# Optimization experiments

Measured on AMD Instinct MI355X. Metric: run time of the kernel, lower is better.

The kernel has to match this reference:

```python
import jax, jax.numpy as jnp
import numpy as np

T, B, N, F = 128, 8, 32, 128
H = 256  # hidden channels
DEG = 8


def setup_inputs() -> dict:
    key = jax.random.key(0)
    ks = jax.random.split(key, 8)
    data = jax.random.normal(ks[0], (T, B, N, F), jnp.float32)
    all_ohs = jax.random.normal(ks[1], (T, B, N, 8), jnp.float32)
    n0 = B * N * T
    n1 = B * N * (T // 2)
    edge_index0 = jax.random.randint(ks[2], (2, n0 * DEG), 0, n0)
    edge_index1 = jax.random.randint(ks[3], (2, n1 * DEG), 0, n1)
    def init(k, shape, fan):
        return jax.random.normal(k, shape, jnp.float32) / np.float32(np.sqrt(fan))
    W0 = init(ks[4], (2 * F, H), 2 * F); b0 = jnp.zeros((H,), jnp.float32)
    Wc0 = init(ks[5], (H, H, 5), H * 5); bc0 = jnp.zeros((H,), jnp.float32)
    W1 = init(ks[6], (2 * H, H), 2 * H); b1 = jnp.zeros((H,), jnp.float32)
    Wc1 = init(ks[7], (H, H, 5), H * 5); bc1 = jnp.zeros((H,), jnp.float32)
    return dict(data=data, all_ohs=all_ohs,
                edge_index0=edge_index0, edge_index1=edge_index1,
                W0=W0, b0=b0, Wc0=Wc0, bc0=bc0,
                W1=W1, b1=b1, Wc1=Wc1, bc1=bc1)


def edge_conv(x, edge_index, W, b):
    # PyG EdgeConv: out_i = max_{(j->i)} relu(Linear(cat[x_i, x_j - x_i]))
    src, dst = edge_index[0], edge_index[1]
    x_i = x[dst]           # [E, C] target features
    x_j = x[src]           # [E, C] source features
    msg = jax.nn.relu(jnp.concatenate([x_i, x_j - x_i], axis=-1) @ W + b)
    out = jax.ops.segment_max(msg, dst, num_segments=x.shape[0])
    return jnp.where(jnp.isneginf(out), 0.0, out)  # empty segments -> 0 (PyG fill)


def temp_conv(x, Wc, bc):
    # x: [BN, C, L]; Conv1d(k=5, pad=2) + relu + MaxPool1d(2)
    y = jax.lax.conv_general_dilated(x, Wc, (1,), [(2, 2)],
                                     dimension_numbers=('NCH', 'OIH', 'NCH'))
    y = jax.nn.relu(y + bc[None, :, None])
    L2 = y.shape[-1] // 2
    y = y[..., : L2 * 2].reshape(y.shape[0], y.shape[1], L2, 2)
    return jnp.max(y, axis=-1)


def reference(data, all_ohs, edge_index0, edge_index1,
              W0, b0, Wc0, bc0, W1, b1, Wc1, bc1):
    # 'fast' path, context=False: all_ohs unused beyond reshape
    length = data.shape[0]
    x = data.reshape(T, B * N, F).transpose(1, 0, 2).reshape(-1, F)  # [BN*T, F]
    layers = ((edge_index0, W0, b0, Wc0, bc0),
              (edge_index1, W1, b1, Wc1, bc1))
    for ei, W, b, Wc, bc in layers:
        x = edge_conv(x, ei, W, b)                       # [BN*length, C]
        x = x.reshape(-1, length, x.shape[-1])           # [BN, length, C]
        x = x.transpose(0, 2, 1)                         # [BN, C, length]
        x = temp_conv(x, Wc, bc)                         # [BN, C, length//2]
        length = x.shape[2]
        C = x.shape[1]
        x = x.transpose(0, 2, 1).reshape(-1, C)          # [BN*length, C]
    return x
```

## Files before the change

### kernel.cpp

```cpp
#include <hip/hip_runtime.h>
#include <hip/hip_bf16.h>
#include <math.h>

#define T0 128
#define BN 256
#define Ff 128
#define Hh 256
#define NODE0 32768
#define E0 262144
#define T1 64
#define NODE1 16384
#define E1 131072
#define CAP 48

typedef __attribute__((ext_vector_type(8))) short bhalf8;
typedef __attribute__((ext_vector_type(4))) float floatx4;
typedef __attribute__((ext_vector_type(16))) float floatx16;

__device__ __forceinline__ unsigned short f2bf(float x) {
  union { float f; unsigned u; } v; v.f = x;
  unsigned r = v.u + 0x7fff + ((v.u >> 16) & 1);
  return (unsigned short)(r >> 16);
}
__device__ __forceinline__ float bf2f(unsigned short b) {
  union { unsigned u; float f; } v; v.u = ((unsigned)b) << 16;
  return v.f;
}
__device__ __forceinline__ void max2(float& mlo, float& mhi, int p) {
  union { unsigned u; float f; } lo, hi;
  lo.u = ((unsigned)p) << 16;
  hi.u = ((unsigned)p) & 0xffff0000u;
  mlo = fmaxf(mlo, lo.f);
  mhi = fmaxf(mhi, hi.f);
}

__global__ void k_prepfill(const float* __restrict__ data, unsigned short* __restrict__ X0b,
                           const float* __restrict__ W0, unsigned short* __restrict__ Wbot0,
                           unsigned short* __restrict__ Wd0,
                           const float* __restrict__ W1, unsigned short* __restrict__ Wbot1,
                           unsigned short* __restrict__ Wd1,
                           const float* __restrict__ Wc0, unsigned short* __restrict__ Wtb0,
                           const float* __restrict__ Wc1, unsigned short* __restrict__ Wtb1,
                           const int* __restrict__ ei0, const int* __restrict__ ei1,
                           int* __restrict__ cnt0, int* __restrict__ cnt1,
                           int* __restrict__ slot0, int* __restrict__ slot1) {
  int b = blockIdx.x;
  int tid = threadIdx.x;
  if (b < 2048) {
    int idx = b * 256 + tid;
    int c8 = idx & 15;
    int r  = idx >> 4;
    int t  = r & (T0 - 1);
    int bn = r >> 7;
    const float* s = data + ((size_t)t * BN + bn) * Ff + c8 * 8;
    float4 a = *(const float4*)s;
    float4 bb = *(const float4*)(s + 4);
    unsigned short o[8];
    o[0] = f2bf(a.x); o[1] = f2bf(a.y); o[2] = f2bf(a.z); o[3] = f2bf(a.w);
    o[4] = f2bf(bb.x); o[5] = f2bf(bb.y); o[6] = f2bf(bb.z); o[7] = f2bf(bb.w);
    *(int4*)(X0b + ((size_t)(bn * T0 + t) * Ff + c8 * 8)) = *(int4*)o;
  } else if (b < 2176) {
    int idx = (b - 2048) * 256 + tid;
    int n = idx >> 7, k = idx & 127;
    float top = W0[(size_t)k * 256 + n];
    float bot = W0[(size_t)(128 + k) * 256 + n];
    Wbot0[idx] = f2bf(bot);
    Wd0[idx]   = f2bf(top - bot);
  } else if (b < 2432) {
    int idx = (b - 2176) * 256 + tid;
    int n = idx >> 8, k = idx & 255;
    float top = W1[(size_t)k * 256 + n];
    float bot = W1[(size_t)(256 + k) * 256 + n];
    Wbot1[idx] = f2bf(bot);
    Wd1[idx]   = f2bf(top - bot);
  } else if (b < 3712) {
    int idx = (b - 2432) * 256 + tid;
    int tap = idx >> 16, o = (idx >> 8) & 255, i = idx & 255;
    Wtb0[idx] = f2bf(Wc0[((size_t)o * 256 + i) * 5 + tap]);
  } else if (b < 4992) {
    int idx = (b - 3712) * 256 + tid;
    int tap = idx >> 16, o = (idx >> 8) & 255, i = idx & 255;
    Wtb1[idx] = f2bf(Wc1[((size_t)o * 256 + i) * 5 + tap]);
  } else {
    int e = (b - 4992) * 256 + tid;
    if (e < E0) {
      int d = ei0[E0 + e];
      int p = atomicAdd(&cnt0[d], 1);
      if (p < CAP) slot0[(size_t)d * CAP + p] = ei0[e];
    } else {
      int e2 = e - E0;
      int d = ei1[E1 + e2];
      int p = atomicAdd(&cnt1[d], 1);
      if (p < CAP) slot1[(size_t)d * CAP + p] = ei1[e2];
    }
  }
}

__global__ __launch_bounds__(256) void k_gemm2(const unsigned short* __restrict__ A,
                                               const unsigned short* __restrict__ Wbot,
                                               const unsigned short* __restrict__ Wd,
                                               unsigned short* __restrict__ Bm,
                                               unsigned short* __restrict__ P, int K,
                                               const float* __restrict__ bias) {
  __shared__ __align__(16) short A_lds[128 * 72];
  __shared__ __align__(16) short B0_lds[128 * 72];
  __shared__ __align__(16) short B1_lds[128 * 72];
  int tid = threadIdx.x;
  int row0 = blockIdx.x * 128;
  int col0 = blockIdx.y * 128;
  int lane = tid & 63, wv = tid >> 6;
  int m16 = lane & 15, quad = lane >> 4;
  int sr = tid >> 3, sseg = tid & 7;

  const unsigned short* Abase  = A    + (size_t)(row0 + sr) * K + sseg * 8;
  const unsigned short* B0base = Wbot + (size_t)(col0 + sr) * K + sseg * 8;
  const unsigned short* B1base = Wd   + (size_t)(col0 + sr) * K + sseg * 8;

  int4 ra[4], rb0[4], rb1[4];
#pragma unroll
  for (int i = 0; i < 4; ++i) {
    ra[i]  = *(const int4*)(Abase  + (size_t)i * 32 * K);
    rb0[i] = *(const int4*)(B0base + (size_t)i * 32 * K);
    rb1[i] = *(const int4*)(B1base + (size_t)i * 32 * K);
  }

  floatx4 accB[2][8], accP[2][8];
#pragma unroll
  for (int rt = 0; rt < 2; ++rt)
#pragma unroll
    for (int nt = 0; nt < 8; ++nt) {
      accB[rt][nt] = (floatx4){0.f, 0.f, 0.f, 0.f};
      accP[rt][nt] = (floatx4){0.f, 0.f, 0.f, 0.f};
    }

  for (int kb = 0; kb < K; kb += 64) {
    __syncthreads();
#pragma unroll
    for (int i = 0; i < 4; ++i) {
      int r = sr + i * 32;
      *(int4*)&A_lds[r * 72 + sseg * 8]  = ra[i];
      *(int4*)&B0_lds[r * 72 + sseg * 8] = rb0[i];
      *(int4*)&B1_lds[r * 72 + sseg * 8] = rb1[i];
    }
    if (kb + 64 < K) {
#pragma unroll
      for (int i = 0; i < 4; ++i) {
        ra[i]  = *(const int4*)(Abase  + (size_t)i * 32 * K + kb + 64);
        rb0[i] = *(const int4*)(B0base + (size_t)i * 32 * K + kb + 64);
        rb1[i] = *(const int4*)(B1base + (size_t)i * 32 * K + kb + 64);
      }
    }
    __syncthreads();
#pragma unroll
    for (int ks = 0; ks < 2; ++ks) {
      bhalf8 a0 = *(const bhalf8*)&A_lds[(wv * 32 + m16) * 72 + ks * 32 + quad * 8];
      bhalf8 a1 = *(const bhalf8*)&A_lds[(wv * 32 + 16 + m16) * 72 + ks * 32 + quad * 8];
#pragma unroll
      for (int nt = 0; nt < 8; ++nt) {
        bhalf8 b0 = *(const bhalf8*)&B0_lds[(nt * 16 + m16) * 72 + ks * 32 + quad * 8];
        accB[0][nt] = __builtin_amdgcn_mfma_f32_16x16x32_bf16(b0, a0, accB[0][nt], 0, 0, 0);
        accB[1][nt] = __builtin_amdgcn_mfma_f32_16x16x32_bf16(b0, a1, accB[1][nt], 0, 0, 0);
        bhalf8 b1 = *(const bhalf8*)&B1_lds[(nt * 16 + m16) * 72 + ks * 32 + quad * 8];
        accP[0][nt] = __builtin_amdgcn_mfma_f32_16x16x32_bf16(b1, a0, accP[0][nt], 0, 0, 0);
        accP[1][nt] = __builtin_amdgcn_mfma_f32_16x16x32_bf16(b1, a1, accP[1][nt], 0, 0, 0);
      }
    }
  }

#pragma unroll
  for (int rt = 0; rt < 2; ++rt) {
    int row = row0 + wv * 32 + rt * 16 + m16;
#pragma unroll
    for (int nt = 0; nt < 8; ++nt) {
      int c = col0 + nt * 16 + quad * 4;
      float4 bv = *(const float4*)&bias[c];
      ushort4 ob, op;
      ob.x = f2bf(accB[rt][nt][0]); ob.y = f2bf(accB[rt][nt][1]);
      ob.z = f2bf(accB[rt][nt][2]); ob.w = f2bf(accB[rt][nt][3]);
      op.x = f2bf(accP[rt][nt][0] + bv.x); op.y = f2bf(accP[rt][nt][1] + bv.y);
      op.z = f2bf(accP[rt][nt][2] + bv.z); op.w = f2bf(accP[rt][nt][3] + bv.w);
      *(ushort4*)(Bm + (size_t)row * 256 + c) = ob;
      *(ushort4*)(P  + (size_t)row * 256 + c) = op;
    }
  }
}

__global__ __launch_bounds__(256) void k_maxg2(const unsigned short* __restrict__ Bm,
                                               const int* __restrict__ cnt,
                                               const int* __restrict__ slot,
                                               const unsigned short* __restrict__ P,
                                               unsigned short* __restrict__ X1) {
  int node = blockIdx.x * 4 + (threadIdx.x >> 6);
  int lane = threadIdx.x & 63;
  int half = lane >> 5, c8 = lane & 31;
  int n = cnt[node];
  if (n > CAP) n = CAP;
  const int* sl = slot + (size_t)node * CAP;
  float m[8];
#pragma unroll
  for (int e = 0; e < 8; ++e) m[e] = -INFINITY;
  for (int i = 0; i < n; i += 8) {
    int s[4];
#pragma unroll
    for (int j = 0; j < 4; ++j) {
      int idx = i + 2 * j + half;
      s[j] = sl[(idx < n) ? idx : (n - 1)];
    }
    int4 v[4];
#pragma unroll
    for (int j = 0; j < 4; ++j)
      v[j] = *(const int4*)(Bm + (size_t)s[j] * 256 + c8 * 8);
#pragma unroll
    for (int j = 0; j < 4; ++j) {
      max2(m[0], m[1], v[j].x);
      max2(m[2], m[3], v[j].y);
      max2(m[4], m[5], v[j].z);
      max2(m[6], m[7], v[j].w);
    }
  }
#pragma unroll
  for (int e = 0; e < 8; ++e) m[e] = fmaxf(m[e], __shfl_xor(m[e], 32));
  if (half == 0) {
    int4 p = *(const int4*)(P + (size_t)node * 256 + c8 * 8);
    int4 o;
    unsigned short r0, r1;
    r0 = f2bf(fmaxf(bf2f((unsigned short)(p.x & 0xffff)) + m[0], 0.f));
    r1 = f2bf(fmaxf(bf2f((unsigned short)((unsigned)p.x >> 16)) + m[1], 0.f));
    o.x = (int)r0 | ((int)r1 << 16);
    r0 = f2bf(fmaxf(bf2f((unsigned short)(p.y & 0xffff)) + m[2], 0.f));
    r1 = f2bf(fmaxf(bf2f((unsigned short)((unsigned)p.y >> 16)) + m[3], 0.f));
    o.y = (int)r0 | ((int)r1 << 16);
    r0 = f2bf(fmaxf(bf2f((unsigned short)(p.z & 0xffff)) + m[4], 0.f));
    r1 = f2bf(fmaxf(bf2f((unsigned short)((unsigned)p.z >> 16)) + m[5], 0.f));
    o.z = (int)r0 | ((int)r1 << 16);
    r0 = f2bf(fmaxf(bf2f((unsigned short)(p.w & 0xffff)) + m[6], 0.f));
    r1 = f2bf(fmaxf(bf2f((unsigned short)((unsigned)p.w >> 16)) + m[7], 0.f));
    o.w = (int)r0 | ((int)r1 << 16);
    *(int4*)(X1 + (size_t)node * 256 + c8 * 8) = o;
  }
}

template <int TRows, int NT, bool OUT_F32>
__global__ __launch_bounds__(256) void k_conv32(const unsigned short* __restrict__ X,
                                                const unsigned short* __restrict__ Wtb,
                                                const float* __restrict__ bc,
                                                void* __restrict__ Yout) {
  const int CB = NT * 64;
  __shared__ __align__(16) short A_lds[2 * 68 * 40];
  __shared__ __align__(16) short B_lds[5 * CB * 40];
  int tid = threadIdx.x;
  int row0 = blockIdx.x * 128;
  int col0 = blockIdx.y * CB;
  int lane = tid & 63, wv = tid >> 6;
  int l31 = lane & 31, khalf = lane >> 5;
  int h = wv & 1, cpart = wv >> 1;

  floatx16 acc[2][NT];
#pragma unroll
  for (int rt = 0; rt < 2; ++rt)
#pragma unroll
    for (int ct = 0; ct < NT; ++ct)
#pragma unroll
      for (int r = 0; r < 16; ++r) acc[rt][ct][r] = 0.f;

  for (int kb = 0; kb < 256; kb += 32) {
    __syncthreads();
    for (int u = tid; u < 544; u += 256) {
      int s = (u >= 272) ? 1 : 0;
      int v = u - s * 272;
      int rr = v >> 2, seg = v & 3;
      int base = row0 + s * 64;
      int lo = base & ~(TRows - 1);
      int gr = base + rr - 2;
      int4 val = {0, 0, 0, 0};
      if (gr >= lo && gr < lo + TRows)
        val = *(const int4*)(X + (size_t)gr * 256 + kb + seg * 8);
      *(int4*)&A_lds[(s * 68 + rr) * 40 + seg * 8] = val;
    }
#pragma unroll
    for (int i = 0; i < 5 * NT; ++i) {
      int u = tid + i * 256;
      int r = u >> 2, seg = u & 3;
      int tap = r / CB, col = r % CB;
      *(int4*)&B_lds[r * 40 + seg * 8] =
          *(const int4*)(Wtb + (size_t)tap * 65536 + (size_t)(col0 + col) * 256 + kb + seg * 8);
    }
    __syncthreads();
#pragma unroll
    for (int tap = 0; tap < 5; ++tap) {
#pragma unroll
      for (int ks = 0; ks < 2; ++ks) {
        int ko = ks * 16 + khalf * 8;
        bhalf8 a[2];
#pragma unroll
        for (int rt = 0; rt < 2; ++rt)
          a[rt] = *(const bhalf8*)&A_lds[(h * 68 + rt * 32 + l31 + tap) * 40 + ko];
#pragma unroll
        for (int ct = 0; ct < NT; ++ct) {
          bhalf8 b = *(const bhalf8*)&B_lds[(tap * CB + cpart * NT * 32 + ct * 32 + l31) * 40 + ko];
#pragma unroll
          for (int rt = 0; rt < 2; ++rt)
            acc[rt][ct] = __builtin_amdgcn_mfma_f32_32x32x16_bf16(a[rt], b, acc[rt][ct], 0, 0, 0);
        }
      }
    }
  }

#pragma unroll
  for (int rt = 0; rt < 2; ++rt) {
#pragma unroll
    for (int ct = 0; ct < NT; ++ct) {
      int c = col0 + cpart * NT * 32 + ct * 32 + l31;
      float bv = bc[c];
#pragma unroll
      for (int r = 0; r < 16; r += 2) {
        int rowg = row0 + h * 64 + rt * 32 + 4 * khalf + 8 * (r >> 2) + (r & 3);
        float y0 = fmaxf(acc[rt][ct][r] + bv, 0.f);
        float y1 = fmaxf(acc[rt][ct][r + 1] + bv, 0.f);
        float p = fmaxf(y0, y1);
        int o = rowg >> 1;
        if (OUT_F32) ((float*)Yout)[(size_t)o * 256 + c] = p;
        else ((unsigned short*)Yout)[(size_t)o * 256 + c] = f2bf(p);
      }
    }
  }
}

extern "C" void kernel_launch(void* const* d_in, const int* in_sizes, int n_in,
                              void* d_out, int out_size, void* d_ws, size_t ws_size,
                              hipStream_t stream) {
  const float* data = (const float*)d_in[0];
  const int* ei0 = (const int*)d_in[2];
  const int* ei1 = (const int*)d_in[3];
  const float* W0  = (const float*)d_in[4];
  const float* b0  = (const float*)d_in[5];
  const float* Wc0 = (const float*)d_in[6];
  const float* bc0 = (const float*)d_in[7];
  const float* W1  = (const float*)d_in[8];
  const float* b1  = (const float*)d_in[9];
  const float* Wc1 = (const float*)d_in[10];
  const float* bc1 = (const float*)d_in[11];
  float* out = (float*)d_out;

  char* base = (char*)d_ws;
  size_t off = 0;
  auto alloc = [&](size_t bytes) { void* p = base + off; off += (bytes + 255) & ~(size_t)255; return p; };
  unsigned short* X0b   = (unsigned short*)alloc((size_t)NODE0 * Ff * 2);
  unsigned short* Bm    = (unsigned short*)alloc((size_t)NODE0 * Hh * 2);
  unsigned short* P     = (unsigned short*)alloc((size_t)NODE0 * Hh * 2);
  unsigned short* X1b   = (unsigned short*)alloc((size_t)NODE0 * Hh * 2);
  unsigned short* Y0b   = (unsigned short*)alloc((size_t)NODE1 * Hh * 2);
  unsigned short* Wbot0 = (unsigned short*)alloc(256 * 128 * 2);
  unsigned short* Wd0   = (unsigned short*)alloc(256 * 128 * 2);
  unsigned short* Wbot1 = (unsigned short*)alloc(256 * 256 * 2);
  unsigned short* Wd1   = (unsigned short*)alloc(256 * 256 * 2);
  unsigned short* Wtb0  = (unsigned short*)alloc(5 * 65536 * 2);
  unsigned short* Wtb1  = (unsigned short*)alloc(5 * 65536 * 2);
  int* cnt0  = (int*)alloc(NODE0 * 4);
  int* cnt1  = (int*)alloc(NODE1 * 4);
  int* slot0 = (int*)alloc((size_t)NODE0 * CAP * 4);
  int* slot1 = (int*)alloc((size_t)NODE1 * CAP * 4);

  hipMemsetAsync(cnt0, 0, (NODE0 + NODE1) * sizeof(int), stream);

  k_prepfill<<<6528, 256, 0, stream>>>(data, X0b, W0, Wbot0, Wd0, W1, Wbot1, Wd1,
                                       Wc0, Wtb0, Wc1, Wtb1,
                                       ei0, ei1, cnt0, cnt1, slot0, slot1);

  k_gemm2<<<dim3(NODE0 / 128, 2), 256, 0, stream>>>(X0b, Wbot0, Wd0, Bm, P, 128, b0);
  k_maxg2<<<NODE0 / 4, 256, 0, stream>>>(Bm, cnt0, slot0, P, X1b);
  k_conv32<128, 2, false><<<dim3(NODE0 / 128, 2), 256, 0, stream>>>(X1b, Wtb0, bc0, Y0b);

  k_gemm2<<<dim3(NODE1 / 128, 2), 256, 0, stream>>>(Y0b, Wbot1, Wd1, Bm, P, 256, b1);
  k_maxg2<<<NODE1 / 4, 256, 0, stream>>>(Bm, cnt1, slot1, P, X1b);
  k_conv32<64, 2, true><<<dim3(NODE1 / 128, 2), 256, 0, stream>>>(X1b, Wtb1, bc1, out);
}
```

Measured before the change: 262.7 us.

## Stage GEMM epilogue through LDS for coalesced stores and drop register prefetch

The GEMM epilogue now writes the bf16 Bm and P tiles into shared memory first, then stores them to global memory as full 16-byte rows, instead of scattered 8-byte stores. The register double-buffered global prefetch is removed, so each K step loads straight from global into LDS. This is meant to cut uncoalesced store traffic and register pressure, which may help occupancy. The cost is losing load/compute overlap in the main loop and adding extra barriers in the epilogue.

Measured after the change: 220.0 us, median of 2. -16.3%, faster.

```diff
diff --git a/kernel.cpp b/kernel.cpp
--- a/kernel.cpp
+++ b/kernel.cpp
@@ -102,9 +102,11 @@
                                                unsigned short* __restrict__ Bm,
                                                unsigned short* __restrict__ P, int K,
                                                const float* __restrict__ bias) {
-  __shared__ __align__(16) short A_lds[128 * 72];
-  __shared__ __align__(16) short B0_lds[128 * 72];
-  __shared__ __align__(16) short B1_lds[128 * 72];
+  __shared__ __align__(16) short S_lds[3 * 128 * 72];
+  short* A_lds  = S_lds;
+  short* B0_lds = S_lds + 128 * 72;
+  short* B1_lds = S_lds + 2 * 128 * 72;
+  short* E_lds  = S_lds;
   int tid = threadIdx.x;
   int row0 = blockIdx.x * 128;
   int col0 = blockIdx.y * 128;
@@ -112,18 +114,6 @@
   int m16 = lane & 15, quad = lane >> 4;
   int sr = tid >> 3, sseg = tid & 7;
 
-  const unsigned short* Abase  = A    + (size_t)(row0 + sr) * K + sseg * 8;
-  const unsigned short* B0base = Wbot + (size_t)(col0 + sr) * K + sseg * 8;
-  const unsigned short* B1base = Wd   + (size_t)(col0 + sr) * K + sseg * 8;
-
-  int4 ra[4], rb0[4], rb1[4];
-#pragma unroll
-  for (int i = 0; i < 4; ++i) {
-    ra[i]  = *(const int4*)(Abase  + (size_t)i * 32 * K);
-    rb0[i] = *(const int4*)(B0base + (size_t)i * 32 * K);
-    rb1[i] = *(const int4*)(B1base + (size_t)i * 32 * K);
-  }
-
   floatx4 accB[2][8], accP[2][8];
 #pragma unroll
   for (int rt = 0; rt < 2; ++rt)
@@ -138,17 +128,12 @@
 #pragma unroll
     for (int i = 0; i < 4; ++i) {
       int r = sr + i * 32;
-      *(int4*)&A_lds[r * 72 + sseg * 8]  = ra[i];
-      *(int4*)&B0_lds[r * 72 + sseg * 8] = rb0[i];
-      *(int4*)&B1_lds[r * 72 + sseg * 8] = rb1[i];
-    }
-    if (kb + 64 < K) {
-#pragma unroll
-      for (int i = 0; i < 4; ++i) {
-        ra[i]  = *(const int4*)(Abase  + (size_t)i * 32 * K + kb + 64);
-        rb0[i] = *(const int4*)(B0base + (size_t)i * 32 * K + kb + 64);
-        rb1[i] = *(const int4*)(B1base + (size_t)i * 32 * K + kb + 64);
-      }
+      *(int4*)&A_lds[r * 72 + sseg * 8] =
+          *(const int4*)(A + (size_t)(row0 + r) * K + kb + sseg * 8);
+      *(int4*)&B0_lds[r * 72 + sseg * 8] =
+          *(const int4*)(Wbot + (size_t)(col0 + r) * K + kb + sseg * 8);
+      *(int4*)&B1_lds[r * 72 + sseg * 8] =
+          *(const int4*)(Wd + (size_t)(col0 + r) * K + kb + sseg * 8);
     }
     __syncthreads();
 #pragma unroll
@@ -167,21 +152,50 @@
     }
   }
 
+  const int ESTR = 136;
+  __syncthreads();
+
 #pragma unroll
   for (int rt = 0; rt < 2; ++rt) {
-    int row = row0 + wv * 32 + rt * 16 + m16;
+    int lr = wv * 32 + rt * 16 + m16;
+#pragma unroll
+    for (int nt = 0; nt < 8; ++nt) {
+      ushort4 ob;
+      ob.x = f2bf(accB[rt][nt][0]); ob.y = f2bf(accB[rt][nt][1]);
+      ob.z = f2bf(accB[rt][nt][2]); ob.w = f2bf(accB[rt][nt][3]);
+      *(ushort4*)&E_lds[lr * ESTR + nt * 16 + quad * 4] = ob;
+    }
+  }
+  __syncthreads();
+#pragma unroll
+  for (int i = 0; i < 8; ++i) {
+    int u = tid + i * 256;
+    int r = u >> 4, ch = u & 15;
+    int4 v = *(const int4*)&E_lds[r * ESTR + ch * 8];
+    *(int4*)(Bm + (size_t)(row0 + r) * 256 + col0 + ch * 8) = v;
+  }
+  __syncthreads();
+
+#pragma unroll
+  for (int rt = 0; rt < 2; ++rt) {
+    int lr = wv * 32 + rt * 16 + m16;
 #pragma unroll
     for (int nt = 0; nt < 8; ++nt) {
       int c = col0 + nt * 16 + quad * 4;
       float4 bv = *(const float4*)&bias[c];
-      ushort4 ob, op;
-      ob.x = f2bf(accB[rt][nt][0]); ob.y = f2bf(accB[rt][nt][1]);
-      ob.z = f2bf(accB[rt][nt][2]); ob.w = f2bf(accB[rt][nt][3]);
+      ushort4 op;
       op.x = f2bf(accP[rt][nt][0] + bv.x); op.y = f2bf(accP[rt][nt][1] + bv.y);
       op.z = f2bf(accP[rt][nt][2] + bv.z); op.w = f2bf(accP[rt][nt][3] + bv.w);
-      *(ushort4*)(Bm + (size_t)row * 256 + c) = ob;
-      *(ushort4*)(P  + (size_t)row * 256 + c) = op;
-    }
+      *(ushort4*)&E_lds[lr * ESTR + nt * 16 + quad * 4] = op;
+    }
+  }
+  __syncthreads();
+#pragma unroll
+  for (int i = 0; i < 8; ++i) {
+    int u = tid + i * 256;
+    int r = u >> 4, ch = u & 15;
+    int4 v = *(const int4*)&E_lds[r * ESTR + ch * 8];
+    *(int4*)(P + (size_t)(row0 + r) * 256 + col0 + ch * 8) = v;
   }
 }
 
```
